# Kernel tuning notes

Hardware: AMD Instinct MI355X
Metric: run time of the kernel (lower is better)

## Reference

```python
import jax, jax.numpy as jnp
import numpy as np

WEIGHT_CE = 1.0
WEIGHT_DICE = 1.0
EPS = 1e-10
SMOOTH = 1e-5


def setup_inputs() -> dict:
    key = jax.random.key(0)
    k1, k2 = jax.random.split(key)
    B, N, H, W, D = 2, 8, 128, 128, 128
    logits = jax.random.normal(k1, (B, N, H, W, D), dtype=jnp.float32)
    pred = jax.nn.softmax(logits, axis=1)  # module expects softmaxed preds
    target = jax.random.randint(k2, (B, 1, H, W, D), 0, N, dtype=jnp.int32)
    return {"pred": pred, "target": target}


def reference(pred, target):
    # pred: (B, N, H, W, D) softmax probs; target: (B, 1, H, W, D) int labels
    B, N = pred.shape[0], pred.shape[1]
    t = target[:, 0]  # (B, H, W, D)

    # --- CE part (faithful to the original's cross-batch one-hot bug) ---
    # loss[b2, hwd] = -sum_b sum_c 1[t[b2,hwd]==c] * log(pred[b,c,hwd]+eps)
    logp_sum = jnp.sum(jnp.log(pred + EPS), axis=0)  # (N, H, W, D)
    gathered = jnp.take_along_axis(
        jnp.broadcast_to(logp_sum[None], (B,) + logp_sum.shape),
        t[:, None], axis=1)[:, 0]  # (B, H, W, D)
    celoss = -jnp.mean(gathered) / B

    # --- MONAI DiceLoss(softmax=False, to_onehot_y=True), defaults ---
    oh = (t[:, None] == jnp.arange(N, dtype=t.dtype)[None, :, None, None, None]).astype(pred.dtype)  # (B,N,H,W,D)
    inter = jnp.sum(oh * pred, axis=(2, 3, 4))   # (B, N)
    ground_o = jnp.sum(oh, axis=(2, 3, 4))       # (B, N)
    pred_o = jnp.sum(pred, axis=(2, 3, 4))       # (B, N)
    dice = jnp.mean(1.0 - (2.0 * inter + SMOOTH) / (ground_o + pred_o + SMOOTH))

    return WEIGHT_CE * celoss + WEIGHT_DICE * dice
```

## Files before the change

kernel.cpp:

```cpp
#include <hip/hip_runtime.h>

#define S_VOX (128*128*128)
#define QV (S_VOX/4)
#define CHUNKS 512
#define CHUNK_Q (QV / CHUNKS)
#define EPSF 1e-10f
#define SMOOTHF 1e-5f

#define NACC 49

__device__ __forceinline__ float wave_reduce(float v) {
#pragma unroll
    for (int off = 32; off > 0; off >>= 1)
        v += __shfl_down(v, off, 64);
    return v;
}

__global__ __launch_bounds__(256) void dice_main(const float* __restrict__ pred,
                                                 const int* __restrict__ tgt,
                                                 float* __restrict__ ws) {
    const int chunk = blockIdx.x >> 2;
    const int n0    = (blockIdx.x & 3) * 2;

    const size_t cb = (size_t)chunk * CHUNK_Q;
    const float4* p00 = (const float4*)pred + (size_t)(n0    ) * QV + cb;
    const float4* p01 = (const float4*)pred + (size_t)(n0 + 1) * QV + cb;
    const float4* p10 = (const float4*)pred + (size_t)(n0 + 8) * QV + cb;
    const float4* p11 = (const float4*)pred + (size_t)(n0 + 9) * QV + cb;
    const int4*   t0p = (const int4*)tgt + cb;
    const int4*   t1p = (const int4*)tgt + (size_t)QV + cb;

    float ce = 0.f;
    float inter[4] = {0.f, 0.f, 0.f, 0.f};
    float po[4]    = {0.f, 0.f, 0.f, 0.f};
    int   gc[4]    = {0, 0, 0, 0};

    for (int k = 0; k < 4; ++k) {
        const int i = threadIdx.x + k * 256;
        const float4 q0 = p00[i];
        const float4 q1 = p01[i];
        const float4 q2 = p10[i];
        const float4 q3 = p11[i];
        const int4   ta = t0p[i];
        const int4   tb = t1p[i];

#define VOXEL(pa, pb, pc, pd, u, v)                                     \
        {                                                               \
            const int ua = ((u) == n0);                                 \
            const int ub = ((u) == n0 + 1);                             \
            const int va = ((v) == n0);                                 \
            const int vb = ((v) == n0 + 1);                             \
            inter[0] += ua ? (pa) : 0.f;  gc[0] += ua;                  \
            inter[1] += ub ? (pb) : 0.f;  gc[1] += ub;                  \
            inter[2] += va ? (pc) : 0.f;  gc[2] += va;                  \
            inter[3] += vb ? (pd) : 0.f;  gc[3] += vb;                  \
            ce += (float)(ua + va) * __logf(((pa) + EPSF) * ((pc) + EPSF)); \
            ce += (float)(ub + vb) * __logf(((pb) + EPSF) * ((pd) + EPSF)); \
            po[0] += (pa); po[1] += (pb); po[2] += (pc); po[3] += (pd); \
        }
        VOXEL(q0.x, q1.x, q2.x, q3.x, ta.x, tb.x)
        VOXEL(q0.y, q1.y, q2.y, q3.y, ta.y, tb.y)
        VOXEL(q0.z, q1.z, q2.z, q3.z, ta.z, tb.z)
        VOXEL(q0.w, q1.w, q2.w, q3.w, ta.w, tb.w)
#undef VOXEL
    }

    __shared__ float red[4][13];
    const int lane = threadIdx.x & 63;
    const int wave = threadIdx.x >> 6;
    float acc[13];
    acc[0] = ce;
#pragma unroll
    for (int l = 0; l < 4; l++) {
        acc[1 + l] = inter[l];
        acc[5 + l] = (float)gc[l];
        acc[9 + l] = po[l];
    }
#pragma unroll
    for (int i = 0; i < 13; i++) {
        float v = wave_reduce(acc[i]);
        if (lane == 0) red[wave][i] = v;
    }
    __syncthreads();
    if (threadIdx.x < 13) {
        const int i = threadIdx.x;
        const float s = red[0][i] + red[1][i] + red[2][i] + red[3][i];
        int dst;
        if (i == 0) {
            dst = 0;
        } else {
            const int l = (i - 1) & 3;
            const int plane = ((l >> 1) * 8) + n0 + (l & 1);
            if (i <= 4)      dst = 1  + plane;
            else if (i <= 8) dst = 17 + plane;
            else             dst = 33 + plane;
        }
        atomicAdd(&ws[dst], s);
    }
}

__global__ void dice_finalize(const float* __restrict__ ws, float* __restrict__ out) {
    const int i = threadIdx.x;
    float term = 0.f;
    if (i < 16) {
        float inter = ws[1 + i];
        float g     = ws[17 + i];
        float p     = ws[33 + i];
        term = 1.0f - (2.0f * inter + SMOOTHF) / (g + p + SMOOTHF);
    }
    term = wave_reduce(term);
    if (i == 0) {
        float celoss = -ws[0] / (4.0f * (float)S_VOX);
        out[0] = celoss + term * (1.0f / 16.0f);
    }
}

extern "C" void kernel_launch(void* const* d_in, const int* in_sizes, int n_in,
                              void* d_out, int out_size, void* d_ws, size_t ws_size,
                              hipStream_t stream) {
    const float* pred = (const float*)d_in[0];
    const int*   tgt  = (const int*)d_in[1];
    float* ws  = (float*)d_ws;
    float* out = (float*)d_out;

    hipMemsetAsync(ws, 0, NACC * sizeof(float), stream);
    dice_main<<<CHUNKS * 4, 256, 0, stream>>>(pred, tgt, ws);
    dice_finalize<<<1, 64, 0, stream>>>(ws, out);
}
```

Measured before the change: 232.2 us.

## Use smaller chunks, XCD-aware block mapping, and per-XCD replicated atomic accumulators

Shrinks each block to one float4 iteration per thread, which gives four times as many blocks. Block indices are remapped so consecutive blocks spread across the 8 XCDs while the four channel-pair blocks of a chunk share an XCD, which helps reuse of target data in that XCD's L2. Atomic accumulators are replicated per XCD with a padded stride to reduce cross-die atomic contention, and the finalize kernel sums the replicas. The cost is many more blocks and more total atomics, with less work per block to hide memory latency.

New measurement: 211.0 us. -9.1%, faster.

```diff
diff --git a/kernel.cpp b/kernel.cpp
--- a/kernel.cpp
+++ b/kernel.cpp
@@ -2,12 +2,13 @@
 
 #define S_VOX (128*128*128)
 #define QV (S_VOX/4)
-#define CHUNKS 512
-#define CHUNK_Q (QV / CHUNKS)
+#define CHUNK_Q 256
+#define CHUNKS (QV / CHUNK_Q)
 #define EPSF 1e-10f
 #define SMOOTHF 1e-5f
 
-#define NACC 49
+#define NREP 8
+#define REP_STRIDE 64
 
 __device__ __forceinline__ float wave_reduce(float v) {
 #pragma unroll
@@ -19,8 +20,10 @@
 __global__ __launch_bounds__(256) void dice_main(const float* __restrict__ pred,
                                                  const int* __restrict__ tgt,
                                                  float* __restrict__ ws) {
-    const int chunk = blockIdx.x >> 2;
-    const int n0    = (blockIdx.x & 3) * 2;
+    const int xcd = blockIdx.x & 7;
+    const int s   = blockIdx.x >> 3;
+    const int chunk = xcd + 8 * (s >> 2);
+    const int n0    = (s & 3) * 2;
 
     const size_t cb = (size_t)chunk * CHUNK_Q;
     const float4* p00 = (const float4*)pred + (size_t)(n0    ) * QV + cb;
@@ -30,40 +33,41 @@
     const int4*   t0p = (const int4*)tgt + cb;
     const int4*   t1p = (const int4*)tgt + (size_t)QV + cb;
 
+    const int i = threadIdx.x;
+    const float4 q0 = p00[i];
+    const float4 q1 = p01[i];
+    const float4 q2 = p10[i];
+    const float4 q3 = p11[i];
+    const int4   ta = t0p[i];
+    const int4   tb = t1p[i];
+
     float ce = 0.f;
     float inter[4] = {0.f, 0.f, 0.f, 0.f};
-    float po[4]    = {0.f, 0.f, 0.f, 0.f};
-    int   gc[4]    = {0, 0, 0, 0};
-
-    for (int k = 0; k < 4; ++k) {
-        const int i = threadIdx.x + k * 256;
-        const float4 q0 = p00[i];
-        const float4 q1 = p01[i];
-        const float4 q2 = p10[i];
-        const float4 q3 = p11[i];
-        const int4   ta = t0p[i];
-        const int4   tb = t1p[i];
+    float po[4];
+    int   gc[4] = {0, 0, 0, 0};
+    po[0] = (q0.x + q0.y) + (q0.z + q0.w);
+    po[1] = (q1.x + q1.y) + (q1.z + q1.w);
+    po[2] = (q2.x + q2.y) + (q2.z + q2.w);
+    po[3] = (q3.x + q3.y) + (q3.z + q3.w);
 
 #define VOXEL(pa, pb, pc, pd, u, v)                                     \
-        {                                                               \
-            const int ua = ((u) == n0);                                 \
-            const int ub = ((u) == n0 + 1);                             \
-            const int va = ((v) == n0);                                 \
-            const int vb = ((v) == n0 + 1);                             \
-            inter[0] += ua ? (pa) : 0.f;  gc[0] += ua;                  \
-            inter[1] += ub ? (pb) : 0.f;  gc[1] += ub;                  \
-            inter[2] += va ? (pc) : 0.f;  gc[2] += va;                  \
-            inter[3] += vb ? (pd) : 0.f;  gc[3] += vb;                  \
-            ce += (float)(ua + va) * __logf(((pa) + EPSF) * ((pc) + EPSF)); \
-            ce += (float)(ub + vb) * __logf(((pb) + EPSF) * ((pd) + EPSF)); \
-            po[0] += (pa); po[1] += (pb); po[2] += (pc); po[3] += (pd); \
-        }
-        VOXEL(q0.x, q1.x, q2.x, q3.x, ta.x, tb.x)
-        VOXEL(q0.y, q1.y, q2.y, q3.y, ta.y, tb.y)
-        VOXEL(q0.z, q1.z, q2.z, q3.z, ta.z, tb.z)
-        VOXEL(q0.w, q1.w, q2.w, q3.w, ta.w, tb.w)
+    {                                                                   \
+        const int ua = ((u) == n0);                                     \
+        const int ub = ((u) == n0 + 1);                                 \
+        const int va = ((v) == n0);                                     \
+        const int vb = ((v) == n0 + 1);                                 \
+        inter[0] += ua ? (pa) : 0.f;  gc[0] += ua;                      \
+        inter[1] += ub ? (pb) : 0.f;  gc[1] += ub;                      \
+        inter[2] += va ? (pc) : 0.f;  gc[2] += va;                      \
+        inter[3] += vb ? (pd) : 0.f;  gc[3] += vb;                      \
+        ce += (float)(ua + va) * __logf(((pa) + EPSF) * ((pc) + EPSF)); \
+        ce += (float)(ub + vb) * __logf(((pb) + EPSF) * ((pd) + EPSF)); \
+    }
+    VOXEL(q0.x, q1.x, q2.x, q3.x, ta.x, tb.x)
+    VOXEL(q0.y, q1.y, q2.y, q3.y, ta.y, tb.y)
+    VOXEL(q0.z, q1.z, q2.z, q3.z, ta.z, tb.z)
+    VOXEL(q0.w, q1.w, q2.w, q3.w, ta.w, tb.w)
 #undef VOXEL
-    }
 
     __shared__ float red[4][13];
     const int lane = threadIdx.x & 63;
@@ -77,25 +81,25 @@
         acc[9 + l] = po[l];
     }
 #pragma unroll
-    for (int i = 0; i < 13; i++) {
-        float v = wave_reduce(acc[i]);
-        if (lane == 0) red[wave][i] = v;
+    for (int k = 0; k < 13; k++) {
+        float v = wave_reduce(acc[k]);
+        if (lane == 0) red[wave][k] = v;
     }
     __syncthreads();
     if (threadIdx.x < 13) {
-        const int i = threadIdx.x;
-        const float s = red[0][i] + red[1][i] + red[2][i] + red[3][i];
+        const int k = threadIdx.x;
+        const float sum = red[0][k] + red[1][k] + red[2][k] + red[3][k];
         int dst;
-        if (i == 0) {
+        if (k == 0) {
             dst = 0;
         } else {
-            const int l = (i - 1) & 3;
+            const int l = (k - 1) & 3;
             const int plane = ((l >> 1) * 8) + n0 + (l & 1);
-            if (i <= 4)      dst = 1  + plane;
-            else if (i <= 8) dst = 17 + plane;
+            if (k <= 4)      dst = 1  + plane;
+            else if (k <= 8) dst = 17 + plane;
             else             dst = 33 + plane;
         }
-        atomicAdd(&ws[dst], s);
+        atomicAdd(&ws[xcd * REP_STRIDE + dst], sum);
     }
 }
 
@@ -103,14 +107,21 @@
     const int i = threadIdx.x;
     float term = 0.f;
     if (i < 16) {
-        float inter = ws[1 + i];
-        float g     = ws[17 + i];
-        float p     = ws[33 + i];
+        float inter = 0.f, g = 0.f, p = 0.f;
+#pragma unroll
+        for (int r = 0; r < NREP; r++) {
+            inter += ws[r * REP_STRIDE + 1  + i];
+            g     += ws[r * REP_STRIDE + 17 + i];
+            p     += ws[r * REP_STRIDE + 33 + i];
+        }
         term = 1.0f - (2.0f * inter + SMOOTHF) / (g + p + SMOOTHF);
     }
     term = wave_reduce(term);
     if (i == 0) {
-        float celoss = -ws[0] / (4.0f * (float)S_VOX);
+        float ce = 0.f;
+#pragma unroll
+        for (int r = 0; r < NREP; r++) ce += ws[r * REP_STRIDE];
+        float celoss = -ce / (4.0f * (float)S_VOX);
         out[0] = celoss + term * (1.0f / 16.0f);
     }
 }
@@ -123,7 +134,7 @@
     float* ws  = (float*)d_ws;
     float* out = (float*)d_out;
 
-    hipMemsetAsync(ws, 0, NACC * sizeof(float), stream);
+    hipMemsetAsync(ws, 0, NREP * REP_STRIDE * sizeof(float), stream);
     dice_main<<<CHUNKS * 4, 256, 0, stream>>>(pred, tgt, ws);
     dice_finalize<<<1, 64, 0, stream>>>(ws, out);
 }
```
